# Kernel optimization log

Hardware: AMD Instinct MI355X
Metric: run time of the kernel (lower is better)

The kernel has to match this reference:

```python
import jax, jax.numpy as jnp
import numpy as np

B, T, N, S = 128, 1024, 128, 256
NEG = jnp.float32(-1e30)  # acts as -inf but keeps grads finite


def setup_inputs() -> dict:
    key = jax.random.key(0)
    k1, k2, k3, k4, k5 = jax.random.split(key, 5)
    inputs = jax.random.normal(k1, (B, T, N), dtype=jnp.float32)
    # nn.Parameter inits to zeros; use small noise so transition actually participates
    transition = 0.05 * jax.random.normal(k2, (N, N), dtype=jnp.float32)
    targets = jax.random.randint(k3, (B, S), 0, N)
    input_lengths = jax.random.randint(k4, (B,), T // 2, T + 1).astype(jnp.int32)
    target_lengths = jax.random.randint(k5, (B,), S // 2, S + 1).astype(jnp.int32)
    return {
        "transition": transition,
        "inputs": inputs,
        "targets": targets,
        "input_lengths": input_lengths,
        "target_lengths": target_lengths,
    }


def reference(transition, inputs, targets, input_lengths, target_lengths):
    # ASG loss = FCC (free-running partition) - FAC (forced alignment score),
    # scale_mode='none', reduction='mean'. transition[j, i] = score of label i -> j.
    xs = jnp.moveaxis(inputs, 1, 0)  # (T, B, N)
    ts = jnp.arange(1, T)

    # ---- FCC: alpha[t, b, j] = x[t,b,j] + logsumexp_i(alpha[t-1,b,i] + trans[j,i])
    def fcc_step(alpha, xt):
        x_t, t = xt
        new = x_t + jax.nn.logsumexp(alpha[:, None, :] + transition[None, :, :], axis=-1)
        return jnp.where((t < input_lengths)[:, None], new, alpha), None

    alphaT, _ = jax.lax.scan(fcc_step, xs[0], (xs[1:], ts))
    fcc = jax.nn.logsumexp(alphaT, axis=-1)  # (B,)

    # ---- FAC: beta[t, b, s] over target positions, self/next transitions only
    self_tr = transition[targets, targets]  # (B, S): stay on targets[s]
    prev_lbl = jnp.concatenate([targets[:, :1], targets[:, :-1]], axis=1)
    next_tr = transition[targets, prev_lbl]  # (B, S): targets[s-1] -> targets[s]

    em0 = jnp.take_along_axis(xs[0], targets, axis=1)  # (B, S)
    beta0 = jnp.where(jnp.arange(S)[None, :] == 0, em0, NEG)

    def fac_step(beta, xt):
        x_t, t = xt
        em = jnp.take_along_axis(x_t, targets, axis=1)  # (B, S)
        shifted = jnp.concatenate(
            [jnp.full((B, 1), NEG, dtype=beta.dtype), beta[:, :-1]], axis=1
        )
        new = em + jnp.logaddexp(beta + self_tr, shifted + next_tr)
        return jnp.where((t < input_lengths)[:, None], new, beta), None

    betaT, _ = jax.lax.scan(fac_step, beta0, (xs[1:], ts))
    fac = jnp.take_along_axis(betaT, (target_lengths - 1)[:, None], axis=1)[:, 0]

    return jnp.mean(fcc - fac)
```

## Files before the change

kernel.cpp:

```cpp
#include <hip/hip_runtime.h>
#include <hip/hip_bf16.h>

#define Bb 128
#define Tt 1024
#define Nn 128
#define Ss 256
#define NEGF (-1e30f)
#define D9 9.0f

typedef __attribute__((ext_vector_type(8))) short short8;
typedef __attribute__((ext_vector_type(4))) float f32x4;

__device__ __forceinline__ short bf16b(float f) {
    __hip_bfloat16 h = __float2bfloat16(f);
    return *reinterpret_cast<short*>(&h);
}

__device__ __forceinline__ unsigned int cvt_pk_bf16(float lo, float hi) {
    unsigned int r;
    asm("v_cvt_pk_bf16_f32 %0, %1, %2" : "=v"(r) : "v"(lo), "v"(hi));
    return r;
}

#define LDS_BARRIER() asm volatile("s_waitcnt lgkmcnt(0)\n\ts_barrier" ::: "memory")

#define FCC_STEP(t_, k_)                                                       \
    {                                                                          \
        const int t = (t_);                                                    \
        const int sl = (k_) & 3;                   \
        f32x4 w0 = xs[sl][0], w1 = xs[sl][1];                                  \
        if (!PRE) {                                                            \
            w0[0] = __expf(w0[0] - D9); w0[1] = __expf(w0[1] - D9);            \
            w0[2] = __expf(w0[2] - D9); w0[3] = __expf(w0[3] - D9);            \
            w1[0] = __expf(w1[0] - D9); w1[1] = __expf(w1[1] - D9);            \
            w1[2] = __expf(w1[2] - D9); w1[3] = __expf(w1[3] - D9);            \
        }                                                                      \
        {     \
            int tn = t + 4; if (tn > Tt - 1) tn = Tt - 1;                      \
            const float* gb = wbase + (size_t)tn * TSTR;                       \
            xs[sl][0] = *(const f32x4*)(gb);                                   \
            xs[sl][1] = *(const f32x4*)(gb + MSTR);                            \
        }                                                                      \
        const short* up = &ut[(t - 1) & 1][g][0] + quad * 8;                   \
        short8 bf0 = *(const short8*)(up);                                     \
        short8 bf1 = *(const short8*)(up + 32);                                \
        short8 bf2 = *(const short8*)(up + 64);                                \
        short8 bf3 = *(const short8*)(up + 96);                                \
        f32x4 a0p = {0.f, 0.f, 0.f, 0.f}, a0q = {0.f, 0.f, 0.f, 0.f};          \
        f32x4 a1p = {0.f, 0.f, 0.f, 0.f}, a1q = {0.f, 0.f, 0.f, 0.f};          \
        a0p = __builtin_amdgcn_mfma_f32_16x16x32_bf16(ea[0][0], bf0, a0p, 0, 0, 0); \
        a1p = __builtin_amdgcn_mfma_f32_16x16x32_bf16(ea[1][0], bf0, a1p, 0, 0, 0); \
        a0q = __builtin_amdgcn_mfma_f32_16x16x32_bf16(ea[0][2], bf2, a0q, 0, 0, 0); \
        a1q = __builtin_amdgcn_mfma_f32_16x16x32_bf16(ea[1][2], bf2, a1q, 0, 0, 0); \
        a0p = __builtin_amdgcn_mfma_f32_16x16x32_bf16(ea[0][1], bf1, a0p, 0, 0, 0); \
        a1p = __builtin_amdgcn_mfma_f32_16x16x32_bf16(ea[1][1], bf1, a1p, 0, 0, 0); \
        a0q = __builtin_amdgcn_mfma_f32_16x16x32_bf16(ea[0][3], bf3, a0q, 0, 0, 0); \
        a1q = __builtin_amdgcn_mfma_f32_16x16x32_bf16(ea[1][3], bf3, a1q, 0, 0, 0); \
        if ((k_) == 0) { \
            float m = fmaxf(fmaxf(wred[0][g], wred[1][g]),                     \
                            fmaxf(wred[2][g], wred[3][g]));                    \
            float invm = 1.0f / m;                                             \
            c += __logf(m);                                                    \
            w0 *= invm; w1 *= invm;                                            \
        }                                                                      \
        f32x4 un0 = w0 * (a0p + a0q);                                          \
        f32x4 un1 = w1 * (a1p + a1q);                                          \
        if (t == len - 1) {  \
            float s = (un0[0] + un0[1]) + (un0[2] + un0[3])                    \
                    + (un1[0] + un1[1]) + (un1[2] + un1[3]);                   \
            s += __shfl_xor(s, 16);                                            \
            s += __shfl_xor(s, 32);                                            \
            sfin = s; cfin = c;                                                \
        }                                                                      \
        {                                                                      \
            uint2 o0, o1;                                                      \
            o0.x = cvt_pk_bf16(un0[0], un0[1]); o0.y = cvt_pk_bf16(un0[2], un0[3]); \
            o1.x = cvt_pk_bf16(un1[0], un1[1]); o1.y = cvt_pk_bf16(un1[2], un1[3]); \
            *reinterpret_cast<uint2*>(&ut[t & 1][g][j0_]) = o0;                \
            *reinterpret_cast<uint2*>(&ut[t & 1][g][j0_ + 16]) = o1;           \
        }                                                                      \
        if ((k_) == 7) { \
            float mm = fmaxf(fmaxf(un0[0], un0[1]), fmaxf(un0[2], un0[3]));    \
            mm = fmaxf(mm, fmaxf(fmaxf(un1[0], un1[1]), fmaxf(un1[2], un1[3])));\
            mm = fmaxf(mm, __shfl_xor(mm, 16));                                \
            mm = fmaxf(mm, __shfl_xor(mm, 32));                                \
            if (lane < 16) wred[q][lane] = mm;                                 \
        }                                                                      \
        LDS_BARRIER();                                                         \
    }

#define FAC_STEP(t_, k_)                                                       \
    {                                                                          \
        const int t = (t_);                                                    \
        const int d = ((k_) + 7) & 7;                                          \
        float e0 = em[d][0], e1 = em[d][1], e2 = em[d][2], e3 = em[d][3];      \
        int tn = t + 8; if (tn > Tt - 1) tn = Tt - 1;                          \
        const float* xrow = xb + (size_t)tn * Nn;                              \
        em[d][0] = xrow[tgi[0]]; em[d][1] = xrow[tgi[1]];                      \
        em[d][2] = xrow[tgi[2]]; em[d][3] = xrow[tgi[3]];                      \
        float bup = __shfl_up(bt[3], 1);                                       \
        float prev0 = (lane == 0) ? NEGF : bup;                                \
        float nb[4];                                                           \
        {                                                                      \
            float aa = bt[0] + st[0], bb = prev0 + ntr[0];                     \
            float hi = fmaxf(aa, bb), lo = fminf(aa, bb);                      \
            nb[0] = e0 + hi + __logf(1.0f + __expf(lo - hi));                  \
        }                                                                      \
        {                                                                      \
            float aa = bt[1] + st[1], bb = bt[0] + ntr[1];                     \
            float hi = fmaxf(aa, bb), lo = fminf(aa, bb);                      \
            nb[1] = e1 + hi + __logf(1.0f + __expf(lo - hi));                  \
        }                                                                      \
        {                                                                      \
            float aa = bt[2] + st[2], bb = bt[1] + ntr[2];                     \
            float hi = fmaxf(aa, bb), lo = fminf(aa, bb);                      \
            nb[2] = e2 + hi + __logf(1.0f + __expf(lo - hi));                  \
        }                                                                      \
        {                                                                      \
            float aa = bt[3] + st[3], bb = bt[2] + ntr[3];                     \
            float hi = fmaxf(aa, bb), lo = fminf(aa, bb);                      \
            nb[3] = e3 + hi + __logf(1.0f + __expf(lo - hi));                  \
        }                                                                      \
        if (t < len) {                                                         \
            bt[0] = nb[0]; bt[1] = nb[1]; bt[2] = nb[2]; bt[3] = nb[3];        \
        }                                                                      \
    }

__global__ __launch_bounds__(256) void exp_w_kernel(const float* __restrict__ x,
                                                    float* __restrict__ w) {
    const int nf4 = Bb * Tt * Nn / 4;
    const int stride = gridDim.x * 256;
    for (int f = blockIdx.x * 256 + threadIdx.x; f < nf4; f += stride) {
        const int l    = f & 63;
        const int mt   = (f >> 6) & 1;
        const int qq   = (f >> 7) & 3;
        const int wv   = (f >> 9) & 7;
        const int t    = f >> 12;
        const int b    = (wv << 4) + (l & 15);
        const int j    = (qq << 5) + (mt << 4) + ((l >> 4) << 2);
        f32x4 v = *(const f32x4*)(x + ((size_t)b * Tt + t) * Nn + j);
        f32x4 r;
        r[0] = __expf(v[0] - D9); r[1] = __expf(v[1] - D9);
        r[2] = __expf(v[2] - D9); r[3] = __expf(v[3] - D9);
        *(f32x4*)(w + 4 * (size_t)f) = r;
    }
}

template <bool PRE>
__global__ __launch_bounds__(256, 1) void asg_main(
    const float* __restrict__ trans, const float* __restrict__ x,
    const float* __restrict__ Wm,
    const int* __restrict__ targets, const int* __restrict__ ilen,
    const int* __restrict__ tlen,
    float* __restrict__ fcc_out, float* __restrict__ fac_out)
{
    __shared__ __align__(16) short ut[2][16][136];
    __shared__ float wred[4][16];

    const int tid  = threadIdx.x;
    const int q    = tid >> 6;
    const int lane = tid & 63;

    if (blockIdx.x < 8) {
        const int g    = lane & 15;
        const int quad = lane >> 4;
        const int wv   = blockIdx.x;
        const int b    = (wv << 4) + g;
        const int len  = ilen[b];
        const int j0_  = 32 * q + 4 * quad;

        constexpr int TSTR = PRE ? 16384 : Nn;
        constexpr int MSTR = PRE ? 64 * 4 : 16;
        const float* wbase = PRE
            ? (Wm + (size_t)(((wv << 2) + q) << 1) * 256 + (lane << 2))
            : (x + (size_t)b * (Tt * Nn) + 32 * q + 4 * quad);

        short8 ea[2][4];
        #pragma unroll
        for (int mt = 0; mt < 2; ++mt) {
            const float* tr = trans + (size_t)(32 * q + 16 * mt + g) * Nn + quad * 8;
            #pragma unroll
            for (int kc = 0; kc < 4; ++kc) {
                short8 v;
                #pragma unroll
                for (int jj = 0; jj < 8; ++jj)
                    v[jj] = bf16b(__expf(tr[kc * 32 + jj]));
                ea[mt][kc] = v;
            }
        }

        f32x4 xs[4][2];
        float c = 0.f, sfin = 1.0f, cfin = 0.f;

        {
            f32x4 v0 = *(const f32x4*)(wbase);
            f32x4 v1 = *(const f32x4*)(wbase + MSTR);
            if (!PRE) {
                v0[0]=__expf(v0[0]-D9); v0[1]=__expf(v0[1]-D9);
                v0[2]=__expf(v0[2]-D9); v0[3]=__expf(v0[3]-D9);
                v1[0]=__expf(v1[0]-D9); v1[1]=__expf(v1[1]-D9);
                v1[2]=__expf(v1[2]-D9); v1[3]=__expf(v1[3]-D9);
            }
            uint2 o0, o1;
            o0.x = cvt_pk_bf16(v0[0], v0[1]); o0.y = cvt_pk_bf16(v0[2], v0[3]);
            o1.x = cvt_pk_bf16(v1[0], v1[1]); o1.y = cvt_pk_bf16(v1[2], v1[3]);
            *reinterpret_cast<uint2*>(&ut[0][g][j0_]) = o0;
            *reinterpret_cast<uint2*>(&ut[0][g][j0_ + 16]) = o1;
        }
        #pragma unroll
        for (int k = 1; k <= 4; ++k) {
            const float* rr = wbase + (size_t)k * TSTR;
            xs[k & 3][0] = *(const f32x4*)(rr);
            xs[k & 3][1] = *(const f32x4*)(rr + MSTR);
        }
        __syncthreads();

        #pragma unroll
        for (int k = 1; k < 8; ++k) FCC_STEP(k, k)
        for (int tb = 8; tb < Tt; tb += 8) {
            #pragma unroll
            for (int k = 0; k < 8; ++k) FCC_STEP(tb + k, k)
        }

        if (lane < 16) wred[q][lane] = sfin;
        __syncthreads();
        if (q == 0 && lane < 16) {
            float tot = wred[0][lane] + wred[1][lane] + wred[2][lane] + wred[3][lane];
            fcc_out[(wv << 4) + lane] = cfin + D9 * (float)len + __logf(tot);
        }
    } else {
        const int b   = ((blockIdx.x - 8) << 2) + q;
        const int len = ilen[b];
        const int tl  = tlen[b];
        const float* xb = x + (size_t)b * Tt * Nn;

        int   tgi[4];
        float st[4], ntr[4], bt[4];
        #pragma unroll
        for (int r = 0; r < 4; ++r) {
            const int s = (lane << 2) + r;
            const int tgv = targets[b * Ss + s];
            const int pg  = (s == 0) ? tgv : targets[b * Ss + s - 1];
            tgi[r] = tgv;
            st[r]  = trans[tgv * Nn + tgv];
            ntr[r] = trans[tgv * Nn + pg];
            bt[r]  = (s == 0) ? xb[tgv] : NEGF;
        }
        float em[8][4];
        #pragma unroll
        for (int k = 1; k <= 8; ++k) {
            int tt = k; if (tt > Tt - 1) tt = Tt - 1;
            const float* xrow = xb + (size_t)tt * Nn;
            em[(k - 1) & 7][0] = xrow[tgi[0]];
            em[(k - 1) & 7][1] = xrow[tgi[1]];
            em[(k - 1) & 7][2] = xrow[tgi[2]];
            em[(k - 1) & 7][3] = xrow[tgi[3]];
        }

        #pragma unroll
        for (int k = 1; k < 8; ++k) FAC_STEP(k, k)
        for (int tb = 8; tb < Tt; tb += 8) {
            #pragma unroll
            for (int k = 0; k < 8; ++k) FAC_STEP(tb + k, k)
        }

        #pragma unroll
        for (int r = 0; r < 4; ++r)
            if ((lane << 2) + r == tl - 1) fac_out[b] = bt[r];
    }
}

__global__ __launch_bounds__(128) void reduce_kernel(const float* __restrict__ fcc,
                                                     const float* __restrict__ fac,
                                                     float* __restrict__ out) {
    __shared__ float r2[2];
    int tid = threadIdx.x;
    float v = fcc[tid] - fac[tid];
    #pragma unroll
    for (int o = 32; o > 0; o >>= 1) v += __shfl_xor(v, o);
    if ((tid & 63) == 0) r2[tid >> 6] = v;
    __syncthreads();
    if (tid == 0) out[0] = (r2[0] + r2[1]) * (1.0f / Bb);
}

extern "C" void kernel_launch(void* const* d_in, const int* in_sizes, int n_in,
                              void* d_out, int out_size, void* d_ws, size_t ws_size,
                              hipStream_t stream) {
    const float* trans   = (const float*)d_in[0];
    const float* x       = (const float*)d_in[1];
    const int*   targets = (const int*)d_in[2];
    const int*   ilen    = (const int*)d_in[3];
    const int*   tlen    = (const int*)d_in[4];
    float* out = (float*)d_out;

    float* fcc = (float*)d_ws;
    float* fac = fcc + Bb;
    float* Wm  = (float*)((char*)d_ws + 2048);

    const size_t wbytes = (size_t)Bb * Tt * Nn * sizeof(float);
    const bool pre = ws_size >= wbytes + 2048;

    if (pre) {
        exp_w_kernel<<<2048, 256, 0, stream>>>(x, Wm);
        asg_main<true><<<40, 256, 0, stream>>>(trans, x, Wm, targets, ilen, tlen, fcc, fac);
    } else {
        asg_main<false><<<40, 256, 0, stream>>>(trans, x, x, targets, ilen, tlen, fcc, fac);
    }
    reduce_kernel<<<1, 128, 0, stream>>>(fcc, fac, out);
}
```

Measured before the change: 389.9 us.

## Compute own-wave K chunk from register-permuted state before reading other waves' LDS

Each wave now builds the B-operand fragment for its own 32-column K chunk of the FCC recurrence directly from its freshly computed outputs via ds_bpermute. It can issue that chunk's MFMAs at the start of the next step, ahead of and independent of the cross-wave LDS reads. Only the other three chunks are read from shared memory, with precomputed pointers and transition fragments reordered per wave. The aim is to shorten the critical path after each barrier, at the cost of four extra bpermutes per step and more live registers.

```diff
diff --git a/kernel.cpp b/kernel.cpp
--- a/kernel.cpp
+++ b/kernel.cpp
@@ -28,6 +28,14 @@
     {                                                                          \
         const int t = (t_);                                                    \
         const int sl = (k_) & 3;                   \
+                            \
+        short8 bfA = *(const short8*)(rp[(t - 1) & 1][0]);                     \
+        short8 bfB = *(const short8*)(rp[(t - 1) & 1][1]);                     \
+        short8 bfC = *(const short8*)(rp[(t - 1) & 1][2]);                     \
+               \
+        const f32x4 zz = {0.f, 0.f, 0.f, 0.f};                                 \
+        f32x4 p1_0 = __builtin_amdgcn_mfma_f32_16x16x32_bf16(e_own0, bf_own, zz, 0, 0, 0); \
+        f32x4 p1_1 = __builtin_amdgcn_mfma_f32_16x16x32_bf16(e_own1, bf_own, zz, 0, 0, 0); \
         f32x4 w0 = xs[sl][0], w1 = xs[sl][1];                                  \
         if (!PRE) {                                                            \
             w0[0] = __expf(w0[0] - D9); w0[1] = __expf(w0[1] - D9);            \
@@ -41,21 +49,6 @@
             xs[sl][0] = *(const f32x4*)(gb);                                   \
             xs[sl][1] = *(const f32x4*)(gb + MSTR);                            \
         }                                                                      \
-        const short* up = &ut[(t - 1) & 1][g][0] + quad * 8;                   \
-        short8 bf0 = *(const short8*)(up);                                     \
-        short8 bf1 = *(const short8*)(up + 32);                                \
-        short8 bf2 = *(const short8*)(up + 64);                                \
-        short8 bf3 = *(const short8*)(up + 96);                                \
-        f32x4 a0p = {0.f, 0.f, 0.f, 0.f}, a0q = {0.f, 0.f, 0.f, 0.f};          \
-        f32x4 a1p = {0.f, 0.f, 0.f, 0.f}, a1q = {0.f, 0.f, 0.f, 0.f};          \
-        a0p = __builtin_amdgcn_mfma_f32_16x16x32_bf16(ea[0][0], bf0, a0p, 0, 0, 0); \
-        a1p = __builtin_amdgcn_mfma_f32_16x16x32_bf16(ea[1][0], bf0, a1p, 0, 0, 0); \
-        a0q = __builtin_amdgcn_mfma_f32_16x16x32_bf16(ea[0][2], bf2, a0q, 0, 0, 0); \
-        a1q = __builtin_amdgcn_mfma_f32_16x16x32_bf16(ea[1][2], bf2, a1q, 0, 0, 0); \
-        a0p = __builtin_amdgcn_mfma_f32_16x16x32_bf16(ea[0][1], bf1, a0p, 0, 0, 0); \
-        a1p = __builtin_amdgcn_mfma_f32_16x16x32_bf16(ea[1][1], bf1, a1p, 0, 0, 0); \
-        a0q = __builtin_amdgcn_mfma_f32_16x16x32_bf16(ea[0][3], bf3, a0q, 0, 0, 0); \
-        a1q = __builtin_amdgcn_mfma_f32_16x16x32_bf16(ea[1][3], bf3, a1q, 0, 0, 0); \
         if ((k_) == 0) { \
             float m = fmaxf(fmaxf(wred[0][g], wred[1][g]),                     \
                             fmaxf(wred[2][g], wred[3][g]));                    \
@@ -63,8 +56,15 @@
             c += __logf(m);                                                    \
             w0 *= invm; w1 *= invm;                                            \
         }                                                                      \
-        f32x4 un0 = w0 * (a0p + a0q);                                          \
-        f32x4 un1 = w1 * (a1p + a1q);                                          \
+                  \
+        p1_0 = __builtin_amdgcn_mfma_f32_16x16x32_bf16(eoA0, bfA, p1_0, 0, 0, 0); \
+        p1_1 = __builtin_amdgcn_mfma_f32_16x16x32_bf16(eoA1, bfA, p1_1, 0, 0, 0); \
+        f32x4 p2_0 = __builtin_amdgcn_mfma_f32_16x16x32_bf16(eoB0, bfB, zz, 0, 0, 0); \
+        f32x4 p2_1 = __builtin_amdgcn_mfma_f32_16x16x32_bf16(eoB1, bfB, zz, 0, 0, 0); \
+        f32x4 p3_0 = __builtin_amdgcn_mfma_f32_16x16x32_bf16(eoC0, bfC, zz, 0, 0, 0); \
+        f32x4 p3_1 = __builtin_amdgcn_mfma_f32_16x16x32_bf16(eoC1, bfC, zz, 0, 0, 0); \
+        f32x4 un0 = w0 * ((p1_0 + p2_0) + p3_0);                               \
+        f32x4 un1 = w1 * ((p1_1 + p2_1) + p3_1);                               \
         if (t == len - 1) {  \
             float s = (un0[0] + un0[1]) + (un0[2] + un0[3])                    \
                     + (un1[0] + un1[1]) + (un1[2] + un1[3]);                   \
@@ -72,13 +72,23 @@
             s += __shfl_xor(s, 32);                                            \
             sfin = s; cfin = c;                                                \
         }                                                                      \
-        {                                                                      \
-            uint2 o0, o1;                                                      \
-            o0.x = cvt_pk_bf16(un0[0], un0[1]); o0.y = cvt_pk_bf16(un0[2], un0[3]); \
-            o1.x = cvt_pk_bf16(un1[0], un1[1]); o1.y = cvt_pk_bf16(un1[2], un1[3]); \
-            *reinterpret_cast<uint2*>(&ut[t & 1][g][j0_]) = o0;                \
-            *reinterpret_cast<uint2*>(&ut[t & 1][g][j0_ + 16]) = o1;           \
-        }                                                                      \
+        uint2 o0, o1;                                                          \
+        o0.x = cvt_pk_bf16(un0[0], un0[1]); o0.y = cvt_pk_bf16(un0[2], un0[3]); \
+        o1.x = cvt_pk_bf16(un1[0], un1[1]); o1.y = cvt_pk_bf16(un1[2], un1[3]); \
+        {  \
+           \
+           \
+            unsigned sx = lowhalf ? o0.x : o1.x;                               \
+            unsigned sy = lowhalf ? o0.y : o1.y;                               \
+            union { short8 s8; int i4[4]; } BO;                                \
+            BO.i4[0] = __builtin_amdgcn_ds_bpermute(addrA, (int)sx);           \
+            BO.i4[1] = __builtin_amdgcn_ds_bpermute(addrA, (int)sy);           \
+            BO.i4[2] = __builtin_amdgcn_ds_bpermute(addrB, (int)sx);           \
+            BO.i4[3] = __builtin_amdgcn_ds_bpermute(addrB, (int)sy);           \
+            bf_own = BO.s8;                                                    \
+        }                                                                      \
+        *reinterpret_cast<uint2*>(wp[t & 1]) = o0;                             \
+        *reinterpret_cast<uint2*>(wp[t & 1] + 16) = o1;                        \
         if ((k_) == 7) { \
             float mm = fmaxf(fmaxf(un0[0], un0[1]), fmaxf(un0[2], un0[3]));    \
             mm = fmaxf(mm, fmaxf(fmaxf(un1[0], un1[1]), fmaxf(un1[2], un1[3])));\
@@ -167,7 +177,6 @@
         const int wv   = blockIdx.x;
         const int b    = (wv << 4) + g;
         const int len  = ilen[b];
-        const int j0_  = 32 * q + 4 * quad;
 
         constexpr int TSTR = PRE ? 16384 : Nn;
         constexpr int MSTR = PRE ? 64 * 4 : 16;
@@ -189,7 +198,50 @@
             }
         }
 
+        short8 e_own0, e_own1, eoA0, eoA1, eoB0, eoB1, eoC0, eoC1;
+        int oc0, oc1, oc2;
+        if (q == 0) {
+            e_own0 = ea[0][0]; e_own1 = ea[1][0];
+            eoA0 = ea[0][1]; eoA1 = ea[1][1];
+            eoB0 = ea[0][2]; eoB1 = ea[1][2];
+            eoC0 = ea[0][3]; eoC1 = ea[1][3];
+            oc0 = 32; oc1 = 64; oc2 = 96;
+        } else if (q == 1) {
+            e_own0 = ea[0][1]; e_own1 = ea[1][1];
+            eoA0 = ea[0][0]; eoA1 = ea[1][0];
+            eoB0 = ea[0][2]; eoB1 = ea[1][2];
+            eoC0 = ea[0][3]; eoC1 = ea[1][3];
+            oc0 = 0; oc1 = 64; oc2 = 96;
+        } else if (q == 2) {
+            e_own0 = ea[0][2]; e_own1 = ea[1][2];
+            eoA0 = ea[0][0]; eoA1 = ea[1][0];
+            eoB0 = ea[0][1]; eoB1 = ea[1][1];
+            eoC0 = ea[0][3]; eoC1 = ea[1][3];
+            oc0 = 0; oc1 = 32; oc2 = 96;
+        } else {
+            e_own0 = ea[0][3]; e_own1 = ea[1][3];
+            eoA0 = ea[0][0]; eoA1 = ea[1][0];
+            eoB0 = ea[0][1]; eoB1 = ea[1][1];
+            eoC0 = ea[0][2]; eoC1 = ea[1][2];
+            oc0 = 0; oc1 = 32; oc2 = 64;
+        }
+
+        const short* rp[2][3];
+        short* wp[2];
+        {
+            const short* b0 = &ut[0][g][quad * 8];
+            const short* b1 = &ut[1][g][quad * 8];
+            rp[0][0] = b0 + oc0; rp[0][1] = b0 + oc1; rp[0][2] = b0 + oc2;
+            rp[1][0] = b1 + oc0; rp[1][1] = b1 + oc1; rp[1][2] = b1 + oc2;
+            wp[0] = &ut[0][g][32 * q + 4 * quad];
+            wp[1] = &ut[1][g][32 * q + 4 * quad];
+        }
+        const int  addrA   = ((quad & 1) * 32 + g) * 4;
+        const int  addrB   = addrA + 64;
+        const bool lowhalf = (quad < 2);
+
         f32x4 xs[4][2];
+        short8 bf_own;
         float c = 0.f, sfin = 1.0f, cfin = 0.f;
 
         {
@@ -204,8 +256,18 @@
             uint2 o0, o1;
             o0.x = cvt_pk_bf16(v0[0], v0[1]); o0.y = cvt_pk_bf16(v0[2], v0[3]);
             o1.x = cvt_pk_bf16(v1[0], v1[1]); o1.y = cvt_pk_bf16(v1[2], v1[3]);
-            *reinterpret_cast<uint2*>(&ut[0][g][j0_]) = o0;
-            *reinterpret_cast<uint2*>(&ut[0][g][j0_ + 16]) = o1;
+            {
+                unsigned sx = lowhalf ? o0.x : o1.x;
+                unsigned sy = lowhalf ? o0.y : o1.y;
+                union { short8 s8; int i4[4]; } BO;
+                BO.i4[0] = __builtin_amdgcn_ds_bpermute(addrA, (int)sx);
+                BO.i4[1] = __builtin_amdgcn_ds_bpermute(addrA, (int)sy);
+                BO.i4[2] = __builtin_amdgcn_ds_bpermute(addrB, (int)sx);
+                BO.i4[3] = __builtin_amdgcn_ds_bpermute(addrB, (int)sy);
+                bf_own = BO.s8;
+            }
+            *reinterpret_cast<uint2*>(wp[0]) = o0;
+            *reinterpret_cast<uint2*>(wp[0] + 16) = o1;
         }
         #pragma unroll
         for (int k = 1; k <= 4; ++k) {
```

Result: slower. 457.7 us (+17.4%).
